# Optimization experiments

Measured on AMD Instinct MI355X. Metric: run time of the kernel, lower is better.

The kernel has to match this reference:

```python
import jax, jax.numpy as jnp
import numpy as np

N_NODES = 100000
N_EDGES = 1600000
D = 64


def setup_inputs() -> dict:
    key = jax.random.key(0)
    k1, k2, k3 = jax.random.split(key, 3)
    z = jax.random.normal(k1, (N_NODES, D), dtype=jnp.float32)
    ei = jax.random.randint(k2, (2, N_EDGES), 0, N_NODES, dtype=jnp.int32)
    W = jax.random.normal(k3, (D, D), dtype=jnp.float32) * (1.0 / np.sqrt(D))
    b = jnp.zeros((D,), dtype=jnp.float32)
    return {"z": z, "ei": ei, "W": W, "b": b}


def reference(z, ei, W, b):
    # PyG GCNConv(64,64) with default add_self_loops=True, normalize=True, bias,
    # followed by ReLU (from StructDec.forward).
    N = z.shape[0]
    loops = jnp.arange(N, dtype=ei.dtype)
    src = jnp.concatenate([ei[0], loops])  # [E+N]
    dst = jnp.concatenate([ei[1], loops])  # [E+N]

    # symmetric normalization: deg computed on dst with unit edge weights
    deg = jax.ops.segment_sum(jnp.ones_like(dst, dtype=z.dtype), dst, num_segments=N)
    dinv = jnp.where(deg > 0, jax.lax.rsqrt(deg), 0.0)  # deg >= 1 due to self-loops
    norm = dinv[src] * dinv[dst]  # [E+N]

    # linear transform first (small GEMM), then gather-scale-scatter
    x = z @ W.T  # [N, D]
    msg = x[src] * norm[:, None]  # [E+N, D]
    out = jax.ops.segment_sum(msg, dst, num_segments=N) + b  # [N, D]
    return jax.nn.relu(out)
```

## Files before the change

kernel.cpp:

```cpp
#include <hip/hip_runtime.h>

#define DD 64
#define BSH 7
#define GBKT 128
#define CAP 2560
#define TILE 4096
#define PTHREADS 512
#define MAXBK 1024

__device__ __forceinline__ float bflo(unsigned int u) {
    return __uint_as_float(u << 16);
}
__device__ __forceinline__ float bfhi(unsigned int u) {
    return __uint_as_float(u & 0xffff0000u);
}
__device__ __forceinline__ unsigned short f2bf(float f) {
    unsigned int b = __float_as_uint(f);
    return (unsigned short)((b + 0x7fffu + ((b >> 16) & 1u)) >> 16);
}
__device__ __forceinline__ void acc_row(uint4 r, float4& lo, float4& hi) {
    lo.x += bflo(r.x); lo.y += bfhi(r.x);
    lo.z += bflo(r.y); lo.w += bfhi(r.y);
    hi.x += bflo(r.z); hi.y += bfhi(r.z);
    hi.z += bflo(r.w); hi.w += bfhi(r.w);
}

__global__ void init_k(int* __restrict__ bcur, int NBK) {
    int i = blockIdx.x * blockDim.x + threadIdx.x;
    if (i < NBK) bcur[i] = i * CAP;
}

__global__ __launch_bounds__(PTHREADS) void part_k(const int* __restrict__ src,
                                                   const int* __restrict__ dst,
                                                   int* __restrict__ bcur,
                                                   int* __restrict__ bp,
                                                   int E, int NBK) {
    __shared__ int hist[MAXBK];
    __shared__ int scanb[MAXBK];
    __shared__ int gbase[MAXBK];
    __shared__ int stage[TILE];
    __shared__ unsigned short bstage[TILE];

    int tid = threadIdx.x;
    int tbase = blockIdx.x * TILE;
    int n = E - tbase;
    if (n > TILE) n = TILE;

    for (int i = tid; i < NBK; i += PTHREADS) hist[i] = 0;
    __syncthreads();

    int pv[TILE / PTHREADS];
    int pb[TILE / PTHREADS];
    #pragma unroll
    for (int e = 0; e < TILE / PTHREADS; ++e) {
        int i = tid + e * PTHREADS;
        pb[e] = -1;
        if (i < n) {
            int s = src[tbase + i];
            int d = dst[tbase + i];
            pv[e] = (s << BSH) | (d & (GBKT - 1));
            pb[e] = d >> BSH;
            atomicAdd(&hist[pb[e]], 1);
        }
    }
    __syncthreads();

    if (tid < 64) {
        int run = 0;
        for (int base = 0; base < NBK; base += 64) {
            int i = base + tid;
            int orig = (i < NBK) ? hist[i] : 0;
            int v = orig;
            #pragma unroll
            for (int off = 1; off < 64; off <<= 1) {
                int t = __shfl_up(v, off, 64);
                if (tid >= off) v += t;
            }
            if (i < NBK) scanb[i] = run + v - orig;
            run += __shfl(v, 63, 64);
        }
    }
    __syncthreads();

    for (int i = tid; i < NBK; i += PTHREADS)
        if (hist[i]) gbase[i] = atomicAdd(&bcur[i], hist[i]);
    __syncthreads();
    for (int i = tid; i < NBK; i += PTHREADS) hist[i] = scanb[i];
    __syncthreads();

    #pragma unroll
    for (int e = 0; e < TILE / PTHREADS; ++e) {
        if (pb[e] >= 0) {
            int r = atomicAdd(&hist[pb[e]], 1);
            stage[r] = pv[e];
            bstage[r] = (unsigned short)pb[e];
        }
    }
    __syncthreads();

    for (int i = tid; i < n; i += PTHREADS) {
        int b = bstage[i];
        bp[gbase[b] + (i - scanb[b])] = stage[i];
    }
}

__global__ void nodedeg_k(const int* __restrict__ bp, const int* __restrict__ bcur,
                          float* __restrict__ dinv, int N) {
    __shared__ int cnt[GBKT];
    int k = blockIdx.x;
    int tid = threadIdx.x;
    int ebeg = k * CAP;
    int eend = bcur[k];
    if (tid < GBKT) cnt[tid] = 0;
    __syncthreads();
    for (int i = ebeg + tid; i < eend; i += 256)
        atomicAdd(&cnt[bp[i] & (GBKT - 1)], 1);
    __syncthreads();
    if (tid < GBKT) {
        int node = (k << BSH) + tid;
        if (node < N) dinv[node] = rsqrtf((float)(1 + cnt[tid]));
    }
}

__global__ __launch_bounds__(512) void gemm_k(const float* __restrict__ z,
                                              const float* __restrict__ W,
                                              const float* __restrict__ dinv,
                                              ushort4* __restrict__ ybf, int N) {
    __shared__ float Wt[64 * 68];
    __shared__ float zt[32 * 68];
    int tid = threadIdx.x;
    for (int i = tid; i < DD * DD; i += 512) {
        int d = i >> 6, k = i & 63;
        Wt[k * 68 + d] = W[i];
    }
    {
        int zr = blockIdx.x * 32 + (tid >> 4);
        float4 v = (zr < N) ? reinterpret_cast<const float4*>(z)[(size_t)zr * 16 + (tid & 15)]
                            : make_float4(0.f, 0.f, 0.f, 0.f);
        *reinterpret_cast<float4*>(&zt[(tid >> 4) * 68 + (tid & 15) * 4]) = v;
    }
    __syncthreads();
    int r = tid >> 4;
    int c = tid & 15;
    int row = blockIdx.x * 32 + r;
    float4 acc = make_float4(0.f, 0.f, 0.f, 0.f);
    #pragma unroll
    for (int k = 0; k < DD; ++k) {
        float zv = zt[r * 68 + k];
        float4 w = *reinterpret_cast<const float4*>(&Wt[k * 68 + c * 4]);
        acc.x = fmaf(zv, w.x, acc.x);
        acc.y = fmaf(zv, w.y, acc.y);
        acc.z = fmaf(zv, w.z, acc.z);
        acc.w = fmaf(zv, w.w, acc.w);
    }
    if (row < N) {
        float s = dinv[row];
        ushort4 o;
        o.x = f2bf(acc.x * s);
        o.y = f2bf(acc.y * s);
        o.z = f2bf(acc.z * s);
        o.w = f2bf(acc.w * s);
        ybf[(size_t)row * 16 + c] = o;
    }
}

__global__ __launch_bounds__(512) void bg_k(const uint4* __restrict__ ybf,
                                            const int* __restrict__ bp,
                                            const int* __restrict__ bcur,
                                            const float4* __restrict__ b4,
                                            float4* __restrict__ out4, int N) {
    __shared__ int cnt[GBKT];
    __shared__ int excl[GBKT];
    __shared__ int cur[GBKT];
    __shared__ int sorted[CAP];
    __shared__ int nextn;
    int k = blockIdx.x;
    int tid = threadIdx.x;
    int ebeg = k * CAP;
    int eend = bcur[k];
    int base = k << BSH;

    if (tid < GBKT) cnt[tid] = 0;
    if (tid == 0) nextn = 0;
    __syncthreads();
    for (int i = ebeg + tid; i < eend; i += 512)
        atomicAdd(&cnt[bp[i] & (GBKT - 1)], 1);
    __syncthreads();

    if (tid < GBKT) excl[tid] = cnt[tid];
    __syncthreads();
    #pragma unroll
    for (int off = 1; off < GBKT; off <<= 1) {
        int t = (tid < GBKT && tid >= off) ? excl[tid - off] : 0;
        __syncthreads();
        if (tid < GBKT) excl[tid] += t;
        __syncthreads();
    }
    if (tid < GBKT) {
        excl[tid] -= cnt[tid];
        cur[tid] = excl[tid];
    }
    __syncthreads();

    for (int i = ebeg + tid; i < eend; i += 512) {
        int v = bp[i];
        int l = v & (GBKT - 1);
        int pos = atomicAdd(&cur[l], 1);
        sorted[pos] = v >> BSH;
    }
    __syncthreads();

    int lane = tid & 63;
    int c = tid & 7;
    for (;;) {
        int slot;
        if ((tid & 7) == 0) slot = atomicAdd(&nextn, 1);
        slot = __shfl(slot, lane & 56, 64);
        if (slot >= GBKT) break;
        int node = base + slot;
        if (node >= N) continue;
        int beg = excl[slot];
        int cn = cnt[slot];
        int end = beg + cn;
        uint4 v = ybf[(size_t)node * 8 + c];
        float4 a0 = make_float4(bflo(v.x), bfhi(v.x), bflo(v.y), bfhi(v.y));
        float4 a1 = make_float4(bflo(v.z), bfhi(v.z), bflo(v.w), bfhi(v.w));
        float4 e0 = make_float4(0.f, 0.f, 0.f, 0.f);
        float4 e1 = e0;
        int j = beg;
        for (; j + 7 < end; j += 8) {
            int s0 = sorted[j],     s1 = sorted[j + 1], s2 = sorted[j + 2], s3 = sorted[j + 3];
            int s4 = sorted[j + 4], s5 = sorted[j + 5], s6 = sorted[j + 6], s7 = sorted[j + 7];
            uint4 r0 = ybf[(size_t)s0 * 8 + c];
            uint4 r1 = ybf[(size_t)s1 * 8 + c];
            uint4 r2 = ybf[(size_t)s2 * 8 + c];
            uint4 r3 = ybf[(size_t)s3 * 8 + c];
            uint4 r4 = ybf[(size_t)s4 * 8 + c];
            uint4 r5 = ybf[(size_t)s5 * 8 + c];
            uint4 r6 = ybf[(size_t)s6 * 8 + c];
            uint4 r7 = ybf[(size_t)s7 * 8 + c];
            acc_row(r0, a0, a1);
            acc_row(r1, e0, e1);
            acc_row(r2, a0, a1);
            acc_row(r3, e0, e1);
            acc_row(r4, a0, a1);
            acc_row(r5, e0, e1);
            acc_row(r6, a0, a1);
            acc_row(r7, e0, e1);
        }
        for (; j + 3 < end; j += 4) {
            int s0 = sorted[j], s1 = sorted[j + 1], s2 = sorted[j + 2], s3 = sorted[j + 3];
            uint4 r0 = ybf[(size_t)s0 * 8 + c];
            uint4 r1 = ybf[(size_t)s1 * 8 + c];
            uint4 r2 = ybf[(size_t)s2 * 8 + c];
            uint4 r3 = ybf[(size_t)s3 * 8 + c];
            acc_row(r0, a0, a1);
            acc_row(r1, e0, e1);
            acc_row(r2, a0, a1);
            acc_row(r3, e0, e1);
        }
        for (; j < end; ++j) {
            uint4 r = ybf[(size_t)sorted[j] * 8 + c];
            acc_row(r, a0, a1);
        }
        a0.x += e0.x; a0.y += e0.y; a0.z += e0.z; a0.w += e0.w;
        a1.x += e1.x; a1.y += e1.y; a1.z += e1.z; a1.w += e1.w;

        float dn = rsqrtf((float)(1 + cn));
        float4 bb0 = b4[2 * c];
        float4 bb1 = b4[2 * c + 1];
        float4 o0, o1;
        o0.x = fmaxf(fmaf(a0.x, dn, bb0.x), 0.f);
        o0.y = fmaxf(fmaf(a0.y, dn, bb0.y), 0.f);
        o0.z = fmaxf(fmaf(a0.z, dn, bb0.z), 0.f);
        o0.w = fmaxf(fmaf(a0.w, dn, bb0.w), 0.f);
        o1.x = fmaxf(fmaf(a1.x, dn, bb1.x), 0.f);
        o1.y = fmaxf(fmaf(a1.y, dn, bb1.y), 0.f);
        o1.z = fmaxf(fmaf(a1.z, dn, bb1.z), 0.f);
        o1.w = fmaxf(fmaf(a1.w, dn, bb1.w), 0.f);
        out4[(size_t)node * 16 + 2 * c] = o0;
        out4[(size_t)node * 16 + 2 * c + 1] = o1;
    }
}


extern "C" void kernel_launch(void* const* d_in, const int* in_sizes, int n_in,
                              void* d_out, int out_size, void* d_ws, size_t ws_size,
                              hipStream_t stream) {
    const float* z = (const float*)d_in[0];
    const int* ei  = (const int*)d_in[1];
    const float* W = (const float*)d_in[2];
    const float* b = (const float*)d_in[3];
    float* out = (float*)d_out;

    const int N = in_sizes[0] / DD;
    const int E = in_sizes[1] / 2;
    const int* src = ei;
    const int* dst = ei + E;

    const int NBK = (N + GBKT - 1) >> BSH;

    unsigned short* ybf = (unsigned short*)d_ws;
    float* dinv  = (float*)(ybf + (size_t)64 * N);
    int*   bcur  = (int*)(dinv + N);
    int*   bp    = bcur + NBK;

    init_k<<<(NBK + 255) / 256, 256, 0, stream>>>(bcur, NBK);
    part_k<<<(E + TILE - 1) / TILE, PTHREADS, 0, stream>>>(src, dst, bcur, bp, E, NBK);
    nodedeg_k<<<NBK, 256, 0, stream>>>(bp, bcur, dinv, N);
    gemm_k<<<(N + 31) / 32, 512, 0, stream>>>(z, W, dinv, (ushort4*)ybf, N);
    bg_k<<<NBK, 512, 0, stream>>>((const uint4*)ybf, bp, bcur,
                                  (const float4*)b, (float4*)out, N);
}
```

Baseline: 95.73 us.

## Reuse histogram atomic ranks, vectorize edge loads, shrink bucket-gather blocks

In the partition kernel, each edge keeps the rank returned by its histogram atomic, so the second shared-memory atomic pass and two barriers are removed. Edge indices are loaded as int4 vectors, eight per thread. The bucket cursor now stores a relative count zeroed by hipMemsetAsync, which replaces the init kernel launch. The gather kernel runs 256 threads per block and caches its bucket edges in registers, so it reads them from global memory once instead of twice. The cost is more register pressure and a hardcoded assumption that a bucket holds at most ten edges per thread.

```diff
diff --git a/kernel.cpp b/kernel.cpp
--- a/kernel.cpp
+++ b/kernel.cpp
@@ -6,6 +6,7 @@
 #define CAP 2560
 #define TILE 4096
 #define PTHREADS 512
+#define EPT 8
 #define MAXBK 1024
 
 __device__ __forceinline__ float bflo(unsigned int u) {
@@ -23,11 +24,6 @@
     lo.z += bflo(r.y); lo.w += bfhi(r.y);
     hi.x += bflo(r.z); hi.y += bfhi(r.z);
     hi.z += bflo(r.w); hi.w += bfhi(r.w);
-}
-
-__global__ void init_k(int* __restrict__ bcur, int NBK) {
-    int i = blockIdx.x * blockDim.x + threadIdx.x;
-    if (i < NBK) bcur[i] = i * CAP;
 }
 
 __global__ __launch_bounds__(PTHREADS) void part_k(const int* __restrict__ src,
@@ -49,18 +45,32 @@
     for (int i = tid; i < NBK; i += PTHREADS) hist[i] = 0;
     __syncthreads();
 
-    int pv[TILE / PTHREADS];
-    int pb[TILE / PTHREADS];
-    #pragma unroll
-    for (int e = 0; e < TILE / PTHREADS; ++e) {
-        int i = tid + e * PTHREADS;
+    int ss[EPT], dd[EPT];
+    int eb = tid * EPT;
+    bool dal = ((reinterpret_cast<size_t>(dst) & 15) == 0);
+    if (dal && eb + EPT <= n) {
+        const int4* s4 = (const int4*)(src + tbase + eb);
+        const int4* d4 = (const int4*)(dst + tbase + eb);
+        int4 a = s4[0], b2 = s4[1], c4 = d4[0], e4 = d4[1];
+        ss[0] = a.x; ss[1] = a.y; ss[2] = a.z; ss[3] = a.w;
+        ss[4] = b2.x; ss[5] = b2.y; ss[6] = b2.z; ss[7] = b2.w;
+        dd[0] = c4.x; dd[1] = c4.y; dd[2] = c4.z; dd[3] = c4.w;
+        dd[4] = e4.x; dd[5] = e4.y; dd[6] = e4.z; dd[7] = e4.w;
+    } else {
+        #pragma unroll
+        for (int e = 0; e < EPT; ++e) {
+            if (eb + e < n) { ss[e] = src[tbase + eb + e]; dd[e] = dst[tbase + eb + e]; }
+            else dd[e] = -1;
+        }
+    }
+    int pv[EPT], pb[EPT], pr[EPT];
+    #pragma unroll
+    for (int e = 0; e < EPT; ++e) {
         pb[e] = -1;
-        if (i < n) {
-            int s = src[tbase + i];
-            int d = dst[tbase + i];
-            pv[e] = (s << BSH) | (d & (GBKT - 1));
-            pb[e] = d >> BSH;
-            atomicAdd(&hist[pb[e]], 1);
+        if (eb + e < n && dd[e] >= 0) {
+            pv[e] = (ss[e] << BSH) | (dd[e] & (GBKT - 1));
+            pb[e] = dd[e] >> BSH;
+            pr[e] = atomicAdd(&hist[pb[e]], 1);
         }
     }
     __syncthreads();
@@ -83,17 +93,13 @@
     __syncthreads();
 
     for (int i = tid; i < NBK; i += PTHREADS)
-        if (hist[i]) gbase[i] = atomicAdd(&bcur[i], hist[i]);
-    __syncthreads();
-    for (int i = tid; i < NBK; i += PTHREADS) hist[i] = scanb[i];
-    __syncthreads();
-
-    #pragma unroll
-    for (int e = 0; e < TILE / PTHREADS; ++e) {
+        if (hist[i]) gbase[i] = i * CAP + atomicAdd(&bcur[i], hist[i]);
+    #pragma unroll
+    for (int e = 0; e < EPT; ++e) {
         if (pb[e] >= 0) {
-            int r = atomicAdd(&hist[pb[e]], 1);
-            stage[r] = pv[e];
-            bstage[r] = (unsigned short)pb[e];
+            int p = scanb[pb[e]] + pr[e];
+            stage[p] = pv[e];
+            bstage[p] = (unsigned short)pb[e];
         }
     }
     __syncthreads();
@@ -110,7 +116,7 @@
     int k = blockIdx.x;
     int tid = threadIdx.x;
     int ebeg = k * CAP;
-    int eend = bcur[k];
+    int eend = ebeg + bcur[k];
     if (tid < GBKT) cnt[tid] = 0;
     __syncthreads();
     for (int i = ebeg + tid; i < eend; i += 256)
@@ -164,7 +170,7 @@
     }
 }
 
-__global__ __launch_bounds__(512) void bg_k(const uint4* __restrict__ ybf,
+__global__ __launch_bounds__(256) void bg_k(const uint4* __restrict__ ybf,
                                             const int* __restrict__ bp,
                                             const int* __restrict__ bcur,
                                             const float4* __restrict__ b4,
@@ -177,14 +183,21 @@
     int k = blockIdx.x;
     int tid = threadIdx.x;
     int ebeg = k * CAP;
-    int eend = bcur[k];
+    int eend = ebeg + bcur[k];
     int base = k << BSH;
 
     if (tid < GBKT) cnt[tid] = 0;
     if (tid == 0) nextn = 0;
     __syncthreads();
-    for (int i = ebeg + tid; i < eend; i += 512)
-        atomicAdd(&cnt[bp[i] & (GBKT - 1)], 1);
+    int ev[10];
+    #pragma unroll
+    for (int u = 0; u < 10; ++u) {
+        int i = ebeg + tid + u * 256;
+        ev[u] = (i < eend) ? bp[i] : -1;
+    }
+    #pragma unroll
+    for (int u = 0; u < 10; ++u)
+        if (ev[u] >= 0) atomicAdd(&cnt[ev[u] & (GBKT - 1)], 1);
     __syncthreads();
 
     if (tid < GBKT) excl[tid] = cnt[tid];
@@ -202,12 +215,13 @@
     }
     __syncthreads();
 
-    for (int i = ebeg + tid; i < eend; i += 512) {
-        int v = bp[i];
-        int l = v & (GBKT - 1);
-        int pos = atomicAdd(&cur[l], 1);
-        sorted[pos] = v >> BSH;
-    }
+    #pragma unroll
+    for (int u = 0; u < 10; ++u)
+        if (ev[u] >= 0) {
+            int l = ev[u] & (GBKT - 1);
+            int pos = atomicAdd(&cur[l], 1);
+            sorted[pos] = ev[u] >> BSH;
+        }
     __syncthreads();
 
     int lane = tid & 63;
@@ -305,10 +319,10 @@
     int*   bcur  = (int*)(dinv + N);
     int*   bp    = bcur + NBK;
 
-    init_k<<<(NBK + 255) / 256, 256, 0, stream>>>(bcur, NBK);
+    hipMemsetAsync(bcur, 0, sizeof(int) * NBK, stream);
     part_k<<<(E + TILE - 1) / TILE, PTHREADS, 0, stream>>>(src, dst, bcur, bp, E, NBK);
     nodedeg_k<<<NBK, 256, 0, stream>>>(bp, bcur, dinv, N);
     gemm_k<<<(N + 31) / 32, 512, 0, stream>>>(z, W, dinv, (ushort4*)ybf, N);
-    bg_k<<<NBK, 512, 0, stream>>>((const uint4*)ybf, bp, bcur,
+    bg_k<<<NBK, 256, 0, stream>>>((const uint4*)ybf, bp, bcur,
                                   (const float4*)b, (float4*)out, N);
 }
```

Measured after the change: 92.30 us. 1.04x faster.
